# Performance work log

Hardware: AMD Instinct MI355X
Metric: run time of the kernel (lower is better)

## Reference

```python
import jax, jax.numpy as jnp
import numpy as np

B, S, DIM = 4, 2048, 1024
HEADS, HD = 16, DIM // 16
HIDDEN, LEVELS = 4 * DIM, 3
LN_EPS = 1e-5


def setup_inputs() -> dict:
    key = jax.random.key(0)
    ks = jax.random.split(key, 10)
    w = lambda k, shape: (jax.random.normal(k, shape, jnp.float32) * 0.02)
    return {
        "x": jax.random.normal(ks[0], (B, S, DIM), jnp.float32),
        "Wq": w(ks[1], (DIM, DIM)),
        "Wk": w(ks[2], (DIM, DIM)),
        "Wv": w(ks[3], (DIM, DIM)),
        "Wo": w(ks[4], (DIM, DIM)),
        "ln1_g": jnp.ones((DIM,), jnp.float32),
        "ln1_b": jnp.zeros((DIM,), jnp.float32),
        "ln2_g": jnp.ones((DIM,), jnp.float32),
        "ln2_b": jnp.zeros((DIM,), jnp.float32),
        "cms_w1": w(ks[5], (LEVELS, DIM, HIDDEN)),
        "cms_b1": jnp.zeros((LEVELS, HIDDEN), jnp.float32),
        "cms_w2": w(ks[6], (LEVELS, HIDDEN, DIM)),
        "cms_b2": jnp.zeros((LEVELS, DIM), jnp.float32),
    }


def _layer_norm(x, g, b):
    m = jnp.mean(x, axis=-1, keepdims=True)
    v = jnp.var(x, axis=-1, keepdims=True)
    return (x - m) * jax.lax.rsqrt(v + LN_EPS) * g + b


def _linear_attn(h, Wq, Wk, Wv, Wo):
    # h: [B, S, DIM]; feature_map(z) = elu(z) + 1 applied to Q and K
    fm = lambda z: jax.nn.elu(z) + 1.0
    Q = fm(h @ Wq).reshape(B, S, HEADS, HD)
    K = fm(h @ Wk).reshape(B, S, HEADS, HD)
    V = (h @ Wv).reshape(B, S, HEADS, HD)
    # scan over time with fast-weight memory M_t = M_{t-1} + k_t (x) v_t
    Qs = jnp.moveaxis(Q, 1, 0)  # [S, B, H, D]
    Ks = jnp.moveaxis(K, 1, 0)
    Vs = jnp.moveaxis(V, 1, 0)

    def step(carry, qkv):
        mem, ksum = carry  # [B,H,D,D], [B,H,D]
        q, k, v = qkv      # each [B,H,D]
        mem = mem + k[..., :, None] * v[..., None, :]
        ksum = ksum + k
        num = jnp.einsum('bhde,bhd->bhe', mem, q)
        den = jnp.einsum('bhd,bhd->bh', ksum, q)[..., None] + 1e-6
        return (mem, ksum), num / den

    init = (jnp.zeros((B, HEADS, HD, HD), h.dtype),
            jnp.zeros((B, HEADS, HD), h.dtype))
    _, ys = jax.lax.scan(step, init, (Qs, Ks, Vs))  # ys: [S,B,H,D]
    out = jnp.moveaxis(ys, 0, 1).reshape(B, S, DIM)
    return out @ Wo


def _cms(h, w1, b1, w2, b2):
    # Continuum Memory System: chain of LEVELS MLPs (dim->4dim->dim).
    y = h
    for l in range(LEVELS):
        y = jax.nn.gelu(y @ w1[l] + b1[l]) @ w2[l] + b2[l]
    return y


def reference(x, Wq, Wk, Wv, Wo, ln1_g, ln1_b, ln2_g, ln2_b,
              cms_w1, cms_b1, cms_w2, cms_b2):
    x = x + _linear_attn(_layer_norm(x, ln1_g, ln1_b), Wq, Wk, Wv, Wo)
    x = x + _cms(_layer_norm(x, ln2_g, ln2_b), cms_w1, cms_b1, cms_w2, cms_b2)
    return x
```

## Files before the change

### kernel.cpp

```cpp
#include <hip/hip_runtime.h>
#include <stdint.h>
#include <math.h>

#define DIM     1024
#define HID     4096
#define SEQ     2048
#define NB      4
#define NH      16
#define HD      64
#define NCHUNK  32
#define MROWS   8192
#define QSTR    3072

typedef unsigned short ushort_t;
typedef __attribute__((ext_vector_type(8))) short bf16x8;
typedef __attribute__((ext_vector_type(4))) float f32x4;

#define OFF_H    ((size_t)0)
#define OFF_Q    ((size_t)16777216)
#define OFF_P    ((size_t)67108864)
#define OFF_KS   ((size_t)100663296)
#define OFF_X1   ((size_t)101187584)
#define OFF_WQT  ((size_t)134742016)
#define OFF_WOT  ((size_t)141033472)
#define OFF_W1T  ((size_t)143130624)
#define OFF_W2T  ((size_t)168296448)
#define OFF_HIDB OFF_Q + 16777216

__device__ __forceinline__ float b2f(ushort_t u) {
    return __uint_as_float(((unsigned int)u) << 16);
}
__device__ __forceinline__ ushort_t f2b(float f) {
    unsigned int u = __float_as_uint(f);
    u += 0x7FFFu + ((u >> 16) & 1u);
    return (ushort_t)(u >> 16);
}
__device__ __forceinline__ void unpack4(uint2 u, float* f) {
    f[0] = __uint_as_float(u.x << 16);
    f[1] = __uint_as_float(u.x & 0xffff0000u);
    f[2] = __uint_as_float(u.y << 16);
    f[3] = __uint_as_float(u.y & 0xffff0000u);
}
__device__ __forceinline__ float fast_gelu(float x) {
    const float u = x * (1.5957691216057308f + 0.07135481627f * x * x);
    const float e = exp2f(-1.4426950408889634f * u);
    return x * __builtin_amdgcn_rcpf(1.0f + e);
}
__device__ __forceinline__ float fast_elu1(float x) {
    return x > 0.0f ? x + 1.0f : exp2f(1.4426950408889634f * x);
}
__device__ __forceinline__ void ldg16(const ushort_t* g, ushort_t* l) {
    __builtin_amdgcn_global_load_lds(
        (const __attribute__((address_space(1))) void*)g,
        (__attribute__((address_space(3))) void*)l, 16, 0, 0);
}

__global__ void __launch_bounds__(256)
transpose_f32_bf16(const float* __restrict__ src, ushort_t* __restrict__ dst, int R, int C)
{
    __shared__ float t[32][33];
    const int bx = blockIdx.x * 32;
    const int by = blockIdx.y * 32;
    const int tx = threadIdx.x, ty = threadIdx.y;
    #pragma unroll
    for (int i = ty; i < 32; i += 8)
        t[i][tx] = src[(size_t)(by + i) * C + bx + tx];
    __syncthreads();
    #pragma unroll
    for (int i = ty; i < 32; i += 8)
        dst[(size_t)(bx + i) * R + by + tx] = f2b(t[tx][i]);
}

__global__ void __launch_bounds__(256)
ln_fwd(const float* __restrict__ xin, const float* __restrict__ g,
       const float* __restrict__ be, ushort_t* __restrict__ out)
{
    const int row = blockIdx.x, tid = threadIdx.x;
    const float4 f = ((const float4*)(xin + (size_t)row * DIM))[tid];
    float v[4] = {f.x, f.y, f.z, f.w};
    float s  = v[0] + v[1] + v[2] + v[3];
    float ss = v[0]*v[0] + v[1]*v[1] + v[2]*v[2] + v[3]*v[3];
    #pragma unroll
    for (int off = 32; off; off >>= 1) {
        s  += __shfl_down(s, off);
        ss += __shfl_down(ss, off);
    }
    __shared__ float red[2][4];
    const int wave = tid >> 6, lane = tid & 63;
    if (lane == 0) { red[0][wave] = s; red[1][wave] = ss; }
    __syncthreads();
    s  = red[0][0] + red[0][1] + red[0][2] + red[0][3];
    ss = red[1][0] + red[1][1] + red[1][2] + red[1][3];
    const float mean = s * (1.0f / DIM);
    const float var  = ss * (1.0f / DIM) - mean * mean;
    const float rstd = rsqrtf(var + 1e-5f);
    ushort_t o[4];
    #pragma unroll
    for (int i = 0; i < 4; i++) {
        const int col = tid * 4 + i;
        o[i] = f2b((v[i] - mean) * rstd * g[col] + be[col]);
    }
    uint2 u2;
    u2.x = (unsigned int)o[0] | ((unsigned int)o[1] << 16);
    u2.y = (unsigned int)o[2] | ((unsigned int)o[3] << 16);
    *(uint2*)(out + (size_t)row * DIM + tid * 4) = u2;
}

#define ACT_NONE 0
#define ACT_ELU1 1
#define ACT_GELU 2
#define ACT_QKV  3

template<int ACT, bool BIAS, bool RES, bool OUTF32>
__global__ void __launch_bounds__(256, 4)
gemm_bt(const ushort_t* __restrict__ A, const ushort_t* __restrict__ Bt,
        const float* __restrict__ bias, const float* __restrict__ resid,
        void* __restrict__ Cout, int M, int N, int K)
{
    __shared__ __align__(16) ushort_t As[2][128 * 32];
    __shared__ __align__(16) ushort_t Bs[2][128 * 32];
    const int tid  = threadIdx.x;
    const int wave = tid >> 6, lane = tid & 63;
    const int bm = blockIdx.x * 128, bn = blockIdx.y * 128;
    const int wm = (wave >> 1) * 64, wn = (wave & 1) * 64;
    const int srow = tid >> 2;
    const int skp  = (tid & 3) * 8;
    const int mrow = lane & 15, kq = (lane >> 4) * 8;
    const bool qkv_elu = (bn < 2048);

    f32x4 acc[4][4] = {};

    const size_t arow0 = (size_t)(bm + srow)      * K;
    const size_t arow1 = (size_t)(bm + srow + 64) * K;
    const size_t brow0 = (size_t)(bn + srow)      * K;
    const size_t brow1 = (size_t)(bn + srow + 64) * K;

    for (int kt = 0; kt < K; kt += 64) {
        __syncthreads();
        #pragma unroll
        for (int hh = 0; hh < 2; hh++) {
            const int ko = kt + hh * 32;
            ldg16(A  + arow0 + ko + skp, As[hh] + tid * 8);
            ldg16(A  + arow1 + ko + skp, As[hh] + 2048 + tid * 8);
            ldg16(Bt + brow0 + ko + skp, Bs[hh] + tid * 8);
            ldg16(Bt + brow1 + ko + skp, Bs[hh] + 2048 + tid * 8);
        }
        __syncthreads();
        #pragma unroll
        for (int hh = 0; hh < 2; hh++) {
            bf16x8 af[4], bfr[4];
            #pragma unroll
            for (int r = 0; r < 4; r++)
                af[r] = *(const bf16x8*)(As[hh] + (wm + r * 16 + mrow) * 32 + kq);
            #pragma unroll
            for (int c = 0; c < 4; c++)
                bfr[c] = *(const bf16x8*)(Bs[hh] + (wn + c * 16 + mrow) * 32 + kq);
            #pragma unroll
            for (int r = 0; r < 4; r++)
                #pragma unroll
                for (int c = 0; c < 4; c++)
                    acc[r][c] = __builtin_amdgcn_mfma_f32_16x16x32_bf16(af[r], bfr[c], acc[r][c], 0, 0, 0);
        }
    }

    const int cr = (lane >> 4) * 4;
    const int cc = lane & 15;
    #pragma unroll
    for (int r = 0; r < 4; r++) {
        #pragma unroll
        for (int c = 0; c < 4; c++) {
            const int gc = bn + wn + c * 16 + cc;
            const float bv = BIAS ? bias[gc] : 0.0f;
            #pragma unroll
            for (int j = 0; j < 4; j++) {
                const int gr = bm + wm + r * 16 + cr + j;
                float vv = acc[r][c][j] + bv;
                if (ACT == ACT_ELU1) vv = fast_elu1(vv);
                if (ACT == ACT_GELU) vv = fast_gelu(vv);
                if (ACT == ACT_QKV)  vv = qkv_elu ? fast_elu1(vv) : vv;
                const size_t oidx = (size_t)gr * N + gc;
                if (RES) vv += resid[oidx];
                if (OUTF32) ((float*)Cout)[oidx] = vv;
                else        ((ushort_t*)Cout)[oidx] = f2b(vv);
            }
        }
    }
}

__global__ void __launch_bounds__(256)
attn_phase1(const ushort_t* __restrict__ qkv,
            float* __restrict__ P, float* __restrict__ Ksum)
{
    const int c = blockIdx.x, h = blockIdx.y, b = blockIdx.z;
    __shared__ ushort_t Ks[64][68], Vs[64][68];
    const int tid = threadIdx.x;
    const size_t rowbase = (size_t)b * SEQ + c * 64;
    #pragma unroll
    for (int i = 0; i < 4; i++) {
        const int lin = tid + 256 * i;
        const int t = lin >> 4, d4 = (lin & 15) * 4;
        const size_t gidx = (rowbase + t) * QSTR + h * HD + d4;
        *(uint2*)&Ks[t][d4] = *(const uint2*)(qkv + 1024 + gidx);
        *(uint2*)&Vs[t][d4] = *(const uint2*)(qkv + 2048 + gidx);
    }
    __syncthreads();
    const int d0 = (tid >> 4) * 4, e0 = (tid & 15) * 4;
    float acc[4][4] = {};
    for (int t = 0; t < 64; t++) {
        float kf[4], vf[4];
        unpack4(*(const uint2*)&Ks[t][d0], kf);
        unpack4(*(const uint2*)&Vs[t][e0], vf);
        #pragma unroll
        for (int i = 0; i < 4; i++)
            #pragma unroll
            for (int j = 0; j < 4; j++)
                acc[i][j] += kf[i] * vf[j];
    }
    const size_t pbase = (((size_t)b * NH + h) * NCHUNK + c) * 4096;
    #pragma unroll
    for (int i = 0; i < 4; i++) {
        float4 o; o.x = acc[i][0]; o.y = acc[i][1]; o.z = acc[i][2]; o.w = acc[i][3];
        *(float4*)(P + pbase + (size_t)(d0 + i) * 64 + e0) = o;
    }
    if (tid < 64) {
        float a = 0.0f;
        for (int t = 0; t < 64; t++) a += b2f(Ks[t][tid]);
        Ksum[(((size_t)b * NH + h) * NCHUNK + c) * 64 + tid] = a;
    }
}

__global__ void __launch_bounds__(256)
attn_prefix(float* __restrict__ P, float* __restrict__ Ksum)
{
    const int bh = blockIdx.y;
    const int e  = blockIdx.x * 256 + threadIdx.x;
    const size_t base = (size_t)bh * NCHUNK * 4096 + e;
    float acc = 0.0f;
    #pragma unroll
    for (int c = 0; c < NCHUNK; c++) {
        const float t = P[base + (size_t)c * 4096];
        P[base + (size_t)c * 4096] = acc;
        acc += t;
    }
    if (blockIdx.x == 0 && threadIdx.x < 64) {
        const size_t kb = (size_t)bh * NCHUNK * 64 + threadIdx.x;
        float a = 0.0f;
        #pragma unroll
        for (int c = 0; c < NCHUNK; c++) {
            const float t = Ksum[kb + c * 64];
            Ksum[kb + c * 64] = a;
            a += t;
        }
    }
}

__global__ void __launch_bounds__(256)
attn_phase2(const ushort_t* __restrict__ qkv, const float* __restrict__ P,
            const float* __restrict__ Ksum, ushort_t* __restrict__ Out)
{
    const int c = blockIdx.x, h = blockIdx.y, b = blockIdx.z;
    const int tid = threadIdx.x;
    __shared__ ushort_t Qs[64][68], KsB[64][68], VsB[64][68];
    __shared__ float S[64][68];
    __shared__ float Mp[64][64];
    __shared__ float kp[64];
    __shared__ float partial[4][64];
    const size_t rowbase = (size_t)b * SEQ + c * 64;
    const size_t pbase = (((size_t)b * NH + h) * NCHUNK + c) * 4096;
    #pragma unroll
    for (int i = 0; i < 4; i++) {
        const int lin = tid + 256 * i;
        const int t = lin >> 4, d4 = (lin & 15) * 4;
        const size_t gidx = (rowbase + t) * QSTR + h * HD + d4;
        *(uint2*)&Qs[t][d4]  = *(const uint2*)(qkv + gidx);
        *(uint2*)&KsB[t][d4] = *(const uint2*)(qkv + 1024 + gidx);
        *(uint2*)&VsB[t][d4] = *(const uint2*)(qkv + 2048 + gidx);
        *(float4*)&Mp[t][d4] = *(const float4*)(P + pbase + lin * 4);
    }
    if (tid < 64) kp[tid] = Ksum[(((size_t)b * NH + h) * NCHUNK + c) * 64 + tid];
    __syncthreads();

    const int t0 = (tid >> 4) * 4;
    const int c0 = (tid & 15) * 4;

    {
        float accS[4][4] = {};
        for (int d4 = 0; d4 < 64; d4 += 4) {
            float qf[4][4], kf[4][4];
            #pragma unroll
            for (int i = 0; i < 4; i++) {
                unpack4(*(const uint2*)&Qs[t0 + i][d4], qf[i]);
                unpack4(*(const uint2*)&KsB[c0 + i][d4], kf[i]);
            }
            #pragma unroll
            for (int i = 0; i < 4; i++)
                #pragma unroll
                for (int j = 0; j < 4; j++)
                    #pragma unroll
                    for (int dd = 0; dd < 4; dd++)
                        accS[i][j] += qf[i][dd] * kf[j][dd];
        }
        #pragma unroll
        for (int i = 0; i < 4; i++) {
            float4 sv;
            sv.x = (c0 + 0 <= t0 + i) ? accS[i][0] : 0.0f;
            sv.y = (c0 + 1 <= t0 + i) ? accS[i][1] : 0.0f;
            sv.z = (c0 + 2 <= t0 + i) ? accS[i][2] : 0.0f;
            sv.w = (c0 + 3 <= t0 + i) ? accS[i][3] : 0.0f;
            *(float4*)&S[t0 + i][c0] = sv;
        }
    }
    __syncthreads();

    {
        const int t = tid & 63, q = tid >> 6;
        const int base = q * 16;
        float a = 0.0f;
        #pragma unroll
        for (int ii = 0; ii < 16; ii++) a += S[t][base + ii];
        #pragma unroll
        for (int d = 0; d < 16; d++) a += b2f(Qs[t][base + d]) * kp[base + d];
        partial[q][t] = a;
    }
    __syncthreads();

    float acc[4][4] = {};
    for (int ii = 0; ii < 64; ii++) {
        float vf[4];
        unpack4(*(const uint2*)&VsB[ii][c0], vf);
        #pragma unroll
        for (int i = 0; i < 4; i++) {
            const float s = S[t0 + i][ii];
            #pragma unroll
            for (int j = 0; j < 4; j++) acc[i][j] += s * vf[j];
        }
    }
    for (int d = 0; d < 64; d++) {
        const float4 mp = *(const float4*)&Mp[d][c0];
        #pragma unroll
        for (int i = 0; i < 4; i++) {
            const float qv = b2f(Qs[t0 + i][d]);
            acc[i][0] += qv * mp.x; acc[i][1] += qv * mp.y;
            acc[i][2] += qv * mp.z; acc[i][3] += qv * mp.w;
        }
    }
    #pragma unroll
    for (int i = 0; i < 4; i++) {
        const float dent = partial[0][t0 + i] + partial[1][t0 + i] +
                           partial[2][t0 + i] + partial[3][t0 + i] + 1e-6f;
        const float r = 1.0f / dent;
        ushort_t o[4];
        #pragma unroll
        for (int j = 0; j < 4; j++) o[j] = f2b(acc[i][j] * r);
        uint2 u2;
        u2.x = (unsigned int)o[0] | ((unsigned int)o[1] << 16);
        u2.y = (unsigned int)o[2] | ((unsigned int)o[3] << 16);
        *(uint2*)(Out + (rowbase + t0 + i) * DIM + h * HD + c0) = u2;
    }
}

extern "C" void kernel_launch(void* const* d_in, const int* in_sizes, int n_in,
                              void* d_out, int out_size, void* d_ws, size_t ws_size,
                              hipStream_t stream)
{
    const float* x      = (const float*)d_in[0];
    const float* Wq     = (const float*)d_in[1];
    const float* Wk     = (const float*)d_in[2];
    const float* Wv     = (const float*)d_in[3];
    const float* Wo     = (const float*)d_in[4];
    const float* ln1g   = (const float*)d_in[5];
    const float* ln1b   = (const float*)d_in[6];
    const float* ln2g   = (const float*)d_in[7];
    const float* ln2b   = (const float*)d_in[8];
    const float* cw1    = (const float*)d_in[9];
    const float* cb1    = (const float*)d_in[10];
    const float* cw2    = (const float*)d_in[11];
    const float* cb2    = (const float*)d_in[12];

    char* ws = (char*)d_ws;
    ushort_t* h     = (ushort_t*)(ws + OFF_H);
    ushort_t* qkv   = (ushort_t*)(ws + OFF_Q);
    float*    Pb    = (float*)(ws + OFF_P);
    float*    ksb   = (float*)(ws + OFF_KS);
    float*    x1    = (float*)(ws + OFF_X1);
    ushort_t* wqkvt = (ushort_t*)(ws + OFF_WQT);
    ushort_t* wot   = (ushort_t*)(ws + OFF_WOT);
    ushort_t* w1t   = (ushort_t*)(ws + OFF_W1T);
    ushort_t* w2t   = (ushort_t*)(ws + OFF_W2T);
    ushort_t* hid   = (ushort_t*)(ws + OFF_HIDB);
    float*    outp  = (float*)d_out;

    const dim3 tb(32, 8);
    transpose_f32_bf16<<<dim3(32, 32), tb, 0, stream>>>(Wq, wqkvt,                   DIM, DIM);
    transpose_f32_bf16<<<dim3(32, 32), tb, 0, stream>>>(Wk, wqkvt + 1024 * 1024,     DIM, DIM);
    transpose_f32_bf16<<<dim3(32, 32), tb, 0, stream>>>(Wv, wqkvt + 2 * 1024 * 1024, DIM, DIM);
    transpose_f32_bf16<<<dim3(32, 32), tb, 0, stream>>>(Wo, wot, DIM, DIM);
    for (int l = 0; l < 3; l++) {
        transpose_f32_bf16<<<dim3(128, 32), tb, 0, stream>>>(cw1 + (size_t)l * DIM * HID,
                                                             w1t + (size_t)l * HID * DIM, DIM, HID);
        transpose_f32_bf16<<<dim3(32, 128), tb, 0, stream>>>(cw2 + (size_t)l * HID * DIM,
                                                             w2t + (size_t)l * DIM * HID, HID, DIM);
    }

    ln_fwd<<<MROWS, 256, 0, stream>>>(x, ln1g, ln1b, h);

    gemm_bt<ACT_QKV, false, false, false><<<dim3(64, 24), 256, 0, stream>>>(
        h, wqkvt, nullptr, nullptr, qkv, MROWS, QSTR, DIM);

    attn_phase1<<<dim3(NCHUNK, NH, NB), 256, 0, stream>>>(qkv, Pb, ksb);
    attn_prefix<<<dim3(16, 64), 256, 0, stream>>>(Pb, ksb);
    attn_phase2<<<dim3(NCHUNK, NH, NB), 256, 0, stream>>>(qkv, Pb, ksb, h);

    gemm_bt<ACT_NONE, false, true, true><<<dim3(64, 8), 256, 0, stream>>>(h, wot, nullptr, x, x1, MROWS, DIM, DIM);

    ln_fwd<<<MROWS, 256, 0, stream>>>(x1, ln2g, ln2b, h);

    const ushort_t* cur = h;
    for (int l = 0; l < 3; l++) {
        gemm_bt<ACT_GELU, true, false, false><<<dim3(64, 32), 256, 0, stream>>>(
            cur, w1t + (size_t)l * HID * DIM, cb1 + (size_t)l * HID, nullptr, hid, MROWS, HID, DIM);
        if (l < 2) {
            gemm_bt<ACT_NONE, true, false, false><<<dim3(64, 8), 256, 0, stream>>>(
                hid, w2t + (size_t)l * DIM * HID, cb2 + (size_t)l * DIM, nullptr, h, MROWS, DIM, HID);
            cur = h;
        } else {
            gemm_bt<ACT_NONE, true, true, true><<<dim3(64, 8), 256, 0, stream>>>(
                hid, w2t + (size_t)l * DIM * HID, cb2 + (size_t)l * DIM, x1, outp, MROWS, DIM, HID);
        }
    }
    (void)in_sizes; (void)n_in; (void)out_size; (void)ws_size;
}
```

Before: 894.5 us.

## Fuse weight transposes with first LayerNorm and switch GEMM to 32x32x16 MFMA

The ten weight-transpose launches and the first LayerNorm launch are merged into a single prep kernel that dispatches on block index, which removes launch overhead and lets the small kernels run side by side. Separately, the GEMM inner loop moves from 16x16x32 MFMA tiles to 32x32x16 MFMA tiles with 2x2 accumulators per wave. The larger tiles need fewer LDS fragment loads per MFMA, at the cost of a different epilogue index mapping.

```diff
diff --git a/kernel.cpp b/kernel.cpp
--- a/kernel.cpp
+++ b/kernel.cpp
@@ -15,6 +15,7 @@
 typedef unsigned short ushort_t;
 typedef __attribute__((ext_vector_type(8))) short bf16x8;
 typedef __attribute__((ext_vector_type(4))) float f32x4;
+typedef __attribute__((ext_vector_type(16))) float f32x16;
 
 #define OFF_H    ((size_t)0)
 #define OFF_Q    ((size_t)16777216)
@@ -56,19 +57,75 @@
 }
 
 __global__ void __launch_bounds__(256)
-transpose_f32_bf16(const float* __restrict__ src, ushort_t* __restrict__ dst, int R, int C)
-{
-    __shared__ float t[32][33];
-    const int bx = blockIdx.x * 32;
-    const int by = blockIdx.y * 32;
+prep_all(const float* __restrict__ Wq, const float* __restrict__ Wk,
+         const float* __restrict__ Wv, const float* __restrict__ Wo,
+         const float* __restrict__ cw1, const float* __restrict__ cw2,
+         ushort_t* __restrict__ wqkvt, ushort_t* __restrict__ wot,
+         ushort_t* __restrict__ w1t, ushort_t* __restrict__ w2t,
+         const float* __restrict__ x, const float* __restrict__ g,
+         const float* __restrict__ be, ushort_t* __restrict__ hout)
+{
+    const int bid = blockIdx.x;
+    if (bid >= 28672) {
+        const int row = bid - 28672;
+        const int tid = threadIdx.y * 32 + threadIdx.x;
+        const float4 f = ((const float4*)(x + (size_t)row * DIM))[tid];
+        float v[4] = {f.x, f.y, f.z, f.w};
+        float s  = v[0] + v[1] + v[2] + v[3];
+        float ss = v[0]*v[0] + v[1]*v[1] + v[2]*v[2] + v[3]*v[3];
+        #pragma unroll
+        for (int off = 32; off; off >>= 1) {
+            s  += __shfl_down(s, off);
+            ss += __shfl_down(ss, off);
+        }
+        __shared__ float red[2][4];
+        const int wave = tid >> 6, lane = tid & 63;
+        if (lane == 0) { red[0][wave] = s; red[1][wave] = ss; }
+        __syncthreads();
+        s  = red[0][0] + red[0][1] + red[0][2] + red[0][3];
+        ss = red[1][0] + red[1][1] + red[1][2] + red[1][3];
+        const float mean = s * (1.0f / DIM);
+        const float var  = ss * (1.0f / DIM) - mean * mean;
+        const float rstd = rsqrtf(var + 1e-5f);
+        ushort_t o[4];
+        #pragma unroll
+        for (int i = 0; i < 4; i++) {
+            const int col = tid * 4 + i;
+            o[i] = f2b((v[i] - mean) * rstd * g[col] + be[col]);
+        }
+        uint2 u2;
+        u2.x = (unsigned int)o[0] | ((unsigned int)o[1] << 16);
+        u2.y = (unsigned int)o[2] | ((unsigned int)o[3] << 16);
+        *(uint2*)(hout + (size_t)row * DIM + tid * 4) = u2;
+        return;
+    }
+    const float* src; ushort_t* dst; int R, C, tlx, tly;
+    if (bid < 4096) {
+        const int w = bid >> 10, t = bid & 1023;
+        src = (w == 0) ? Wq : (w == 1) ? Wk : (w == 2) ? Wv : Wo;
+        dst = (w < 3) ? (wqkvt + (size_t)w * 1048576) : wot;
+        R = 1024; C = 1024; tlx = t & 31; tly = t >> 5;
+    } else if (bid < 16384) {
+        const int l = (bid - 4096) >> 12, t = (bid - 4096) & 4095;
+        src = cw1 + (size_t)l * DIM * HID;
+        dst = w1t + (size_t)l * HID * DIM;
+        R = 1024; C = 4096; tlx = t & 127; tly = t >> 7;
+    } else {
+        const int l = (bid - 16384) >> 12, t = (bid - 16384) & 4095;
+        src = cw2 + (size_t)l * HID * DIM;
+        dst = w2t + (size_t)l * DIM * HID;
+        R = 4096; C = 1024; tlx = t & 31; tly = t >> 5;
+    }
+    __shared__ float tl[32][33];
+    const int bx = tlx * 32, by = tly * 32;
     const int tx = threadIdx.x, ty = threadIdx.y;
     #pragma unroll
     for (int i = ty; i < 32; i += 8)
-        t[i][tx] = src[(size_t)(by + i) * C + bx + tx];
+        tl[i][tx] = src[(size_t)(by + i) * C + bx + tx];
     __syncthreads();
     #pragma unroll
     for (int i = ty; i < 32; i += 8)
-        dst[(size_t)(bx + i) * R + by + tx] = f2b(t[tx][i]);
+        dst[(size_t)(bx + i) * R + by + tx] = f2b(tl[tx][i]);
 }
 
 __global__ void __launch_bounds__(256)
@@ -125,10 +182,11 @@
     const int wm = (wave >> 1) * 64, wn = (wave & 1) * 64;
     const int srow = tid >> 2;
     const int skp  = (tid & 3) * 8;
-    const int mrow = lane & 15, kq = (lane >> 4) * 8;
+    const int r32 = lane & 31;
+    const int kh  = lane >> 5;
     const bool qkv_elu = (bn < 2048);
 
-    f32x4 acc[4][4] = {};
+    f32x16 acc[2][2] = {};
 
     const size_t arow0 = (size_t)(bm + srow)      * K;
     const size_t arow1 = (size_t)(bm + srow + 64) * K;
@@ -148,33 +206,31 @@
         __syncthreads();
         #pragma unroll
         for (int hh = 0; hh < 2; hh++) {
-            bf16x8 af[4], bfr[4];
-            #pragma unroll
-            for (int r = 0; r < 4; r++)
-                af[r] = *(const bf16x8*)(As[hh] + (wm + r * 16 + mrow) * 32 + kq);
-            #pragma unroll
-            for (int c = 0; c < 4; c++)
-                bfr[c] = *(const bf16x8*)(Bs[hh] + (wn + c * 16 + mrow) * 32 + kq);
-            #pragma unroll
-            for (int r = 0; r < 4; r++)
-                #pragma unroll
-                for (int c = 0; c < 4; c++)
-                    acc[r][c] = __builtin_amdgcn_mfma_f32_16x16x32_bf16(af[r], bfr[c], acc[r][c], 0, 0, 0);
-        }
-    }
-
-    const int cr = (lane >> 4) * 4;
-    const int cc = lane & 15;
-    #pragma unroll
-    for (int r = 0; r < 4; r++) {
-        #pragma unroll
-        for (int c = 0; c < 4; c++) {
-            const int gc = bn + wn + c * 16 + cc;
+            #pragma unroll
+            for (int k16 = 0; k16 < 2; k16++) {
+                const int ko = k16 * 16 + kh * 8;
+                const bf16x8 a0 = *(const bf16x8*)(As[hh] + (wm + r32) * 32 + ko);
+                const bf16x8 a1 = *(const bf16x8*)(As[hh] + (wm + 32 + r32) * 32 + ko);
+                const bf16x8 b0 = *(const bf16x8*)(Bs[hh] + (wn + r32) * 32 + ko);
+                const bf16x8 b1 = *(const bf16x8*)(Bs[hh] + (wn + 32 + r32) * 32 + ko);
+                acc[0][0] = __builtin_amdgcn_mfma_f32_32x32x16_bf16(a0, b0, acc[0][0], 0, 0, 0);
+                acc[0][1] = __builtin_amdgcn_mfma_f32_32x32x16_bf16(a0, b1, acc[0][1], 0, 0, 0);
+                acc[1][0] = __builtin_amdgcn_mfma_f32_32x32x16_bf16(a1, b0, acc[1][0], 0, 0, 0);
+                acc[1][1] = __builtin_amdgcn_mfma_f32_32x32x16_bf16(a1, b1, acc[1][1], 0, 0, 0);
+            }
+        }
+    }
+
+    #pragma unroll
+    for (int mi = 0; mi < 2; mi++) {
+        #pragma unroll
+        for (int ni = 0; ni < 2; ni++) {
+            const int gc = bn + wn + ni * 32 + r32;
             const float bv = BIAS ? bias[gc] : 0.0f;
             #pragma unroll
-            for (int j = 0; j < 4; j++) {
-                const int gr = bm + wm + r * 16 + cr + j;
-                float vv = acc[r][c][j] + bv;
+            for (int reg = 0; reg < 16; reg++) {
+                const int gr = bm + wm + mi * 32 + (reg & 3) + 8 * (reg >> 2) + 4 * kh;
+                float vv = acc[mi][ni][reg] + bv;
                 if (ACT == ACT_ELU1) vv = fast_elu1(vv);
                 if (ACT == ACT_GELU) vv = fast_gelu(vv);
                 if (ACT == ACT_QKV)  vv = qkv_elu ? fast_elu1(vv) : vv;
@@ -390,19 +446,9 @@
     ushort_t* hid   = (ushort_t*)(ws + OFF_HIDB);
     float*    outp  = (float*)d_out;
 
-    const dim3 tb(32, 8);
-    transpose_f32_bf16<<<dim3(32, 32), tb, 0, stream>>>(Wq, wqkvt,                   DIM, DIM);
-    transpose_f32_bf16<<<dim3(32, 32), tb, 0, stream>>>(Wk, wqkvt + 1024 * 1024,     DIM, DIM);
-    transpose_f32_bf16<<<dim3(32, 32), tb, 0, stream>>>(Wv, wqkvt + 2 * 1024 * 1024, DIM, DIM);
-    transpose_f32_bf16<<<dim3(32, 32), tb, 0, stream>>>(Wo, wot, DIM, DIM);
-    for (int l = 0; l < 3; l++) {
-        transpose_f32_bf16<<<dim3(128, 32), tb, 0, stream>>>(cw1 + (size_t)l * DIM * HID,
-                                                             w1t + (size_t)l * HID * DIM, DIM, HID);
-        transpose_f32_bf16<<<dim3(32, 128), tb, 0, stream>>>(cw2 + (size_t)l * HID * DIM,
-                                                             w2t + (size_t)l * DIM * HID, HID, DIM);
-    }
-
-    ln_fwd<<<MROWS, 256, 0, stream>>>(x, ln1g, ln1b, h);
+    prep_all<<<36864, dim3(32, 8), 0, stream>>>(Wq, Wk, Wv, Wo, cw1, cw2,
+                                                wqkvt, wot, w1t, w2t,
+                                                x, ln1g, ln1b, h);
 
     gemm_bt<ACT_QKV, false, false, false><<<dim3(64, 24), 256, 0, stream>>>(
         h, wqkvt, nullptr, nullptr, qkv, MROWS, QSTR, DIM);
```

Result: slower. 936.4 us (+4.7%).
